# Optimization experiments

Hardware: AMD Instinct MI355X
Metric: run time of the kernel (lower is better)

The kernel has to match this reference:

```python
import jax, jax.numpy as jnp
import numpy as np

NUM_HEADS = 8  # from init_kwargs


def setup_inputs() -> dict:
    key = jax.random.key(0)
    ks = jax.random.split(key, 8)
    B, N, Din, H, Dout, E = 4, 2048, 256, 512, 256, 65536
    s = 0.02
    return {
        "x": jax.random.normal(ks[0], (B, N, Din), jnp.float32),
        "edge_index": jax.random.randint(ks[1], (2, E), 0, N),
        "W_gcn": jax.random.normal(ks[2], (Din, H), jnp.float32) * s,
        "b_gcn": jnp.zeros((H,), jnp.float32),
        "in_proj_w": jax.random.normal(ks[3], (3 * H, H), jnp.float32) * s,
        "in_proj_b": jnp.zeros((3 * H,), jnp.float32),
        "out_proj_w": jax.random.normal(ks[4], (H, H), jnp.float32) * s,
        "out_proj_b": jnp.zeros((H,), jnp.float32),
        "fc_w": jax.random.normal(ks[5], (H, Dout), jnp.float32) * s,
        "fc_b": jnp.zeros((Dout,), jnp.float32),
    }


def _gcn(x, edge_index, W, b):
    # PyG GCNConv: add self-loops, symmetric normalization, gather-scatter aggregation.
    B, N, _ = x.shape
    loop = jnp.arange(N)
    src = jnp.concatenate([edge_index[0], loop])  # message source j
    dst = jnp.concatenate([edge_index[1], loop])  # aggregation target i
    deg = jnp.zeros((N,), x.dtype).at[dst].add(1.0)
    dinv = jnp.where(deg > 0, jax.lax.rsqrt(deg), 0.0)
    norm = dinv[src] * dinv[dst]                  # [Etot]
    xl = x @ W                                    # [B, N, H]
    msgs = xl[:, src, :] * norm[None, :, None]    # [B, Etot, H]
    out = jnp.zeros_like(xl).at[:, dst].add(msgs)  # scatter-add over edges
    return out + b


def _mha(x_nbh, wi, bi, wo, bo, nh):
    # torch MultiheadAttention, input [N(seq), B, H], self-attention.
    N, B, H = x_nbh.shape
    dh = H // nh
    qkv = x_nbh @ wi.T + bi                       # [N, B, 3H]
    q, k, v = jnp.split(qkv, 3, axis=-1)
    q = q.reshape(N, B, nh, dh) * (dh ** -0.5)
    k = k.reshape(N, B, nh, dh)
    v = v.reshape(N, B, nh, dh)
    scores = jnp.einsum("nbhd,mbhd->bhnm", q, k)  # [B, nh, N, N]
    attn = jax.nn.softmax(scores, axis=-1)
    o = jnp.einsum("bhnm,mbhd->nbhd", attn, v).reshape(N, B, H)
    return o @ wo.T + bo


def reference(x, edge_index, W_gcn, b_gcn, in_proj_w, in_proj_b,
              out_proj_w, out_proj_b, fc_w, fc_b):
    h = _gcn(x, edge_index, W_gcn, b_gcn)         # [B, N, H]
    h = jnp.transpose(h, (1, 0, 2))               # [N, B, H]
    h = _mha(h, in_proj_w, in_proj_b, out_proj_w, out_proj_b, NUM_HEADS)
    h = jnp.transpose(h, (1, 0, 2))               # [B, N, H]
    h = jax.nn.relu(h)
    return h @ fc_w + fc_b                        # [B, N, Dout]
```

## Files before the change

kernel.cpp:

```cpp
#include <hip/hip_runtime.h>
#include <hip/hip_bf16.h>


#define NN 2048
#define HH 512
#define NHEAD 8
#define DH 64

typedef _Float16 f16;
typedef __attribute__((ext_vector_type(2))) _Float16 f16x2;
typedef __attribute__((ext_vector_type(4))) _Float16 f16x4;
typedef __attribute__((ext_vector_type(8))) _Float16 f16x8;
typedef __attribute__((ext_vector_type(4))) float f32x4;

#define GLOAD_LDS16(g, l)                                              \
  __builtin_amdgcn_global_load_lds(                                    \
      (const __attribute__((address_space(1))) void*)(g),              \
      (__attribute__((address_space(3))) void*)(l), 16, 0, 0)

__device__ __forceinline__ float fast_exp2(float x) {
#if __has_builtin(__builtin_amdgcn_exp2f)
  return __builtin_amdgcn_exp2f(x);
#else
  return exp2f(x);
#endif
}

__device__ __forceinline__ f16x2 cvt_pk_f16(float a, float b) {
#if __has_builtin(__builtin_amdgcn_cvt_pkrtz)
  return __builtin_bit_cast(f16x2, __builtin_amdgcn_cvt_pkrtz(a, b));
#else
  f16x2 r = { (f16)a, (f16)b };
  return r;
#endif
}


__global__ __launch_bounds__(256) void prep_all_kernel(const float* __restrict__ wi,
                                                       const float* __restrict__ wo,
                                                       const float* __restrict__ wg,
                                                       const float* __restrict__ fcw,
                                                       f16* __restrict__ wi16,
                                                       f16* __restrict__ wo16,
                                                       f16* __restrict__ wg16t,
                                                       f16* __restrict__ fcw16t,
                                                       float* __restrict__ deg,
                                                       int* __restrict__ cursor) {
  __shared__ float tbuf[32][33];
  const int bid = blockIdx.x, t = threadIdx.x;
  if (bid < 768) {
    const int i = bid * 256 + t;
    const float4 v = ((const float4*)wi)[i];
    f16x4 o = { (f16)v.x, (f16)v.y, (f16)v.z, (f16)v.w };
    ((f16x4*)wi16)[i] = o;
  } else if (bid < 1024) {
    const int i = (bid - 768) * 256 + t;
    const float4 v = ((const float4*)wo)[i];
    f16x4 o = { (f16)v.x, (f16)v.y, (f16)v.z, (f16)v.w };
    ((f16x4*)wo16)[i] = o;
  } else if (bid == 1024) {
    for (int i = t; i < NN; i += 256) { deg[i] = 0.0f; cursor[i] = 0; }
  } else {
    const int id = bid - 1025;
    const float* in;
    f16* outp;
    int R, C, bx, by;
    if (id < 128) { in = wg;  outp = wg16t;  R = 256; C = 512;
                    bx = id & 15; by = id >> 4; }
    else { int id2 = id - 128; in = fcw; outp = fcw16t; R = 512; C = 256;
           bx = id2 & 7; by = id2 >> 3; }
    const int c0 = bx * 32, r0 = by * 32;
    const int tx = t & 31, ty = t >> 5;
#pragma unroll
    for (int i = 0; i < 32; i += 8) tbuf[ty + i][tx] = in[(size_t)(r0 + ty + i) * C + c0 + tx];
    __syncthreads();
#pragma unroll
    for (int i = 0; i < 32; i += 8)
      outp[(size_t)(c0 + ty + i) * R + r0 + tx] = (f16)tbuf[tx][ty + i];
  }
}


__global__ __launch_bounds__(256) void count_deg_kernel(const int* __restrict__ ei, int E,
                                                        float* __restrict__ deg) {
  int e = blockIdx.x * 256 + threadIdx.x;
  if (e < E) atomicAdd(&deg[ei[E + e]], 1.0f);
}

__global__ __launch_bounds__(1024) void build_rowptr_kernel(const float* __restrict__ deg,
                                                            float* __restrict__ dinv,
                                                            int* __restrict__ rowptr) {
  __shared__ int a[NN];
  __shared__ int bbuf[NN];
  const int t = threadIdx.x;
  for (int i = t; i < NN; i += 1024) {
    float dg = deg[i];
    a[i] = (int)dg;
    dinv[i] = rsqrtf(dg + 1.0f);
  }
  __syncthreads();
  int* src = a;
  int* dst = bbuf;
  for (int off = 1; off < NN; off <<= 1) {
    for (int i = t; i < NN; i += 1024) {
      int v = src[i];
      if (i >= off) v += src[i - off];
      dst[i] = v;
    }
    __syncthreads();
    int* tmp = src; src = dst; dst = tmp;
  }
  for (int i = t; i < NN; i += 1024) rowptr[i + 1] = src[i];
  if (t == 0) rowptr[0] = 0;
}

__global__ __launch_bounds__(256) void fill_csr_kernel(const int* __restrict__ ei, int E,
                                                       const int* __restrict__ rowptr,
                                                       int* __restrict__ cursor,
                                                       int* __restrict__ csr_src) {
  int e = blockIdx.x * 256 + threadIdx.x;
  if (e < E) {
    int s = ei[e];
    int d = ei[E + e];
    int pos = atomicAdd(&cursor[d], 1);
    csr_src[rowptr[d] + pos] = s;
  }
}


template <int OUTMODE, bool BIAS, bool RELU, bool AF32, int MT = 128>
__global__ __launch_bounds__(256) void mfma_gemm_kernel(
    const void* __restrict__ Ap, const f16* __restrict__ Bt,
    const float* __restrict__ bias, void* __restrict__ Cout,
    int M, int N, int K,
    f16* __restrict__ q_out, f16* __restrict__ k_out, f16* __restrict__ v_out) {
  constexpr int MI = MT / 32;
  __shared__ f16 As[MT * 32];
  __shared__ f16 Bs[128 * 32];
  const int tid = threadIdx.x;
  const int wave = tid >> 6, lane = tid & 63;
  const int quad = lane >> 4, l16 = lane & 15;
  const int m0 = blockIdx.y * MT, n0 = blockIdx.x * 128;
  const int moff = (wave >> 1) * (MI * 16), noff = (wave & 1) * 64;

  f32x4 acc[MI][4];
#pragma unroll
  for (int i = 0; i < MI; ++i)
#pragma unroll
    for (int j = 0; j < 4; ++j) acc[i][j] = (f32x4){0.f, 0.f, 0.f, 0.f};

  const int rpw = MT / 4;
  const int srowA = rpw * wave + (lane >> 2);
  const int srowB = 32 * wave + (lane >> 2);
  const int kch = (lane & 3) * 8;
  const f16* Ag = (const f16*)Ap + (size_t)(m0 + srowA) * K + kch;
  const float* Ag32 = (const float*)Ap + (size_t)(m0 + srowA) * K + kch;
  const f16* Bg = Bt + (size_t)(n0 + srowB) * K + kch;
  f16* As_w = &As[(rpw * wave) * 32];
  f16* Bs_w = &Bs[(32 * wave) * 32];

  for (int k0 = 0; k0 < K; k0 += 32) {
    __syncthreads();
    if (AF32) {
#pragma unroll
      for (int t = 0; t < 2; ++t) {
        const float* g = Ag32 + k0 + (size_t)(16 * t) * K;
        const float4 u0 = *(const float4*)g;
        const float4 u1 = *(const float4*)(g + 4);
        f16x8 o = { (f16)u0.x, (f16)u0.y, (f16)u0.z, (f16)u0.w,
                    (f16)u1.x, (f16)u1.y, (f16)u1.z, (f16)u1.w };
        *(f16x8*)&As[(srowA + 16 * t) * 32 + kch] = o;
      }
    } else {
      GLOAD_LDS16(Ag + k0, As_w);
      if (MT == 128) GLOAD_LDS16(Ag + k0 + (size_t)16 * K, As_w + 16 * 32);
    }
    GLOAD_LDS16(Bg + k0, Bs_w);
    GLOAD_LDS16(Bg + k0 + (size_t)16 * K, Bs_w + 16 * 32);
    __syncthreads();
    f16x8 af[MI], bf[4];
#pragma unroll
    for (int m16 = 0; m16 < MI; ++m16)
      af[m16] = *(const f16x8*)&As[(moff + m16 * 16 + l16) * 32 + quad * 8];
#pragma unroll
    for (int n16 = 0; n16 < 4; ++n16)
      bf[n16] = *(const f16x8*)&Bs[(noff + n16 * 16 + l16) * 32 + quad * 8];
#pragma unroll
    for (int m16 = 0; m16 < MI; ++m16)
#pragma unroll
      for (int n16 = 0; n16 < 4; ++n16)
        acc[m16][n16] =
            __builtin_amdgcn_mfma_f32_16x16x32_f16(af[m16], bf[n16], acc[m16][n16], 0, 0, 0);
  }

  float bv[4];
#pragma unroll
  for (int n16 = 0; n16 < 4; ++n16)
    bv[n16] = BIAS ? bias[n0 + noff + n16 * 16 + l16] : 0.f;

  if (OUTMODE == 2) {
    const int hblk = (n0 >> 6) + (wave & 1);
    const int which = hblk >> 3, h = hblk & 7;
    f16* dst = (which == 0) ? q_out : (which == 1) ? k_out : v_out;
    const float scale = (which == 0) ? 0.125f * 1.44269504088896340736f : 1.0f;
#pragma unroll
    for (int m16 = 0; m16 < MI; ++m16) {
#pragma unroll
      for (int r = 0; r < 4; ++r) {
        const int m = m0 + moff + m16 * 16 + quad * 4 + r;
        const int b = m >> 11, ns = m & 2047;
        f16* row = dst + ((size_t)(b * 8 + h) * NN + ns) * DH;
#pragma unroll
        for (int n16 = 0; n16 < 4; ++n16) {
          const int d = n16 * 16 + l16;
          row[d] = (f16)((acc[m16][n16][r] + bv[n16]) * scale);
        }
      }
    }
  } else {
#pragma unroll
    for (int m16 = 0; m16 < MI; ++m16) {
#pragma unroll
      for (int r = 0; r < 4; ++r) {
        const size_t row = (size_t)(m0 + moff + m16 * 16 + quad * 4 + r) * N;
#pragma unroll
        for (int n16 = 0; n16 < 4; ++n16) {
          const int col = n0 + noff + n16 * 16 + l16;
          float v = acc[m16][n16][r] + bv[n16];
          if (RELU) v = fmaxf(v, 0.f);
          if (OUTMODE == 0) ((float*)Cout)[row + col] = v;
          else ((f16*)Cout)[row + col] = (f16)v;
        }
      }
    }
  }
}


__global__ __launch_bounds__(256) void gcn_aggregate_kernel(const f16* __restrict__ xl,
                                                            const float* __restrict__ dinv,
                                                            const int* __restrict__ rowptr,
                                                            const int* __restrict__ csr_src,
                                                            const float* __restrict__ b_gcn,
                                                            f16* __restrict__ out) {
  __shared__ int s_src[256];
  __shared__ float s_dv[256];
  const int i = blockIdx.x;
  const int tid = threadIdx.x;
  const float dv_i = dinv[i];
  const int b = tid >> 6;
  const int f = (tid & 63) * 8;
  const f16* xb = xl + (size_t)(b * NN) * HH + f;
  float acc[8];
  {
    const f16x8 self = *(const f16x8*)&xb[(size_t)i * HH];
#pragma unroll
    for (int j = 0; j < 8; ++j) acc[j] = (float)self[j] * dv_i;
  }
  const int beg = rowptr[i], end = rowptr[i + 1];
  for (int c0 = beg; c0 < end; c0 += 256) {
    const int cnt = min(256, end - c0);
    __syncthreads();
    if (tid < cnt) {
      int s = csr_src[c0 + tid];
      s_src[tid] = s;
      s_dv[tid] = dinv[s];
    }
    __syncthreads();
    for (int t = 0; t < cnt; ++t) {
      const f16x8 v = *(const f16x8*)&xb[(size_t)s_src[t] * HH];
      const float w = s_dv[t];
#pragma unroll
      for (int j = 0; j < 8; ++j) acc[j] = fmaf((float)v[j], w, acc[j]);
    }
  }
  const float4 bg0 = *(const float4*)&b_gcn[f];
  const float4 bg1 = *(const float4*)&b_gcn[f + 4];
  f16x8 o;
  o[0] = (f16)(acc[0] * dv_i + bg0.x);
  o[1] = (f16)(acc[1] * dv_i + bg0.y);
  o[2] = (f16)(acc[2] * dv_i + bg0.z);
  o[3] = (f16)(acc[3] * dv_i + bg0.w);
  o[4] = (f16)(acc[4] * dv_i + bg1.x);
  o[5] = (f16)(acc[5] * dv_i + bg1.y);
  o[6] = (f16)(acc[6] * dv_i + bg1.z);
  o[7] = (f16)(acc[7] * dv_i + bg1.w);
  *(f16x8*)&out[((size_t)(b * NN) + i) * HH + f] = o;
}


__global__ __launch_bounds__(256, 2) void flash_attn_f16_kernel(const f16* __restrict__ Qb,
                                                                const f16* __restrict__ Kb,
                                                                const f16* __restrict__ Vb,
                                                                f16* __restrict__ out) {
  constexpr int LDK = 72;
  constexpr int LDV = 128;
  __shared__ f16 Ks[128 * LDK];
  __shared__ f16 Vt[64 * LDV];
  const int tid = threadIdx.x;
  const int wave = tid >> 6, lane = tid & 63;
  const int quad = lane >> 4, l16 = lane & 15;
  const int bid = blockIdx.x;
  const int sw = (bid & 7) * 64 + (bid >> 3);
  const int bh = sw >> 4;
  const int n0 = (sw & 15) * 128;
  const int b = bh >> 3, h = bh & 7;
  const f16* kb = Kb + (size_t)bh * NN * DH;
  const f16* vb = Vb + (size_t)bh * NN * DH;

  f16x8 aq[2][2];
#pragma unroll
  for (int g = 0; g < 2; ++g) {
    const f16* qf = Qb + ((size_t)bh * NN + n0 + (wave + 4 * g) * 16 + l16) * DH + quad * 8;
    aq[g][0] = *(const f16x8*)qf;
    aq[g][1] = *(const f16x8*)(qf + 32);
  }

  const f16x8 ones = { (f16)1.f, (f16)1.f, (f16)1.f, (f16)1.f,
                       (f16)1.f, (f16)1.f, (f16)1.f, (f16)1.f };

  f32x4 acc_l[2];
  f32x4 acc_o[2][4];
#pragma unroll
  for (int g = 0; g < 2; ++g) {
    acc_l[g] = (f32x4){0.f, 0.f, 0.f, 0.f};
#pragma unroll
    for (int n16 = 0; n16 < 4; ++n16) acc_o[g][n16] = (f32x4){0.f, 0.f, 0.f, 0.f};
  }

  const int kr = tid >> 3, kc = (tid & 7) * 8;
  const int vdg = tid & 15, jbb = tid >> 4;
  int fdr[4];
#pragma unroll
  for (int n16 = 0; n16 < 4; ++n16)
    fdr[n16] = (2 * n16 + l16 + (l16 >> 3)) & 7;

  f16x8 kreg[4];
  f16x4 vreg[2][4];

  auto load_tile = [&](int k0) {
#pragma unroll
    for (int i = 0; i < 4; ++i)
      kreg[i] = *(const f16x8*)(kb + (size_t)(k0 + kr + 32 * i) * DH + kc);
#pragma unroll
    for (int cc = 0; cc < 2; ++cc) {
      const int jb = jbb + 16 * cc;
#pragma unroll
      for (int i = 0; i < 4; ++i)
        vreg[cc][i] = *(const f16x4*)(vb + (size_t)(k0 + jb * 4 + i) * DH + vdg * 4);
    }
  };
  auto store_tile = [&]() {
#pragma unroll
    for (int i = 0; i < 4; ++i)
      *(f16x8*)&Ks[(kr + 32 * i) * LDK + kc] = kreg[i];
#pragma unroll
    for (int cc = 0; cc < 2; ++cc) {
      const int jb = jbb + 16 * cc;
      const int vch = (jb >> 3) * 4 + (jb & 3);
      const int vrem = ((jb >> 2) & 1) * 4;
#pragma unroll
      for (int c = 0; c < 4; ++c) {
        const int d = vdg * 4 + c;
        const int fd = (d + (d >> 3)) & 7;
        const int off = (((vch & 8) | ((vch ^ fd) & 7)) << 3) + vrem;
        f16x4 o = { vreg[cc][0][c], vreg[cc][1][c], vreg[cc][2][c], vreg[cc][3][c] };
        *(f16x4*)&Vt[d * LDV + off] = o;
      }
    }
  };
  auto do_p = [&](int p) {
    f32x4 sA[2][2];
#pragma unroll
    for (int t = 0; t < 2; ++t) {
      const f16x8 ak0 = *(const f16x8*)&Ks[(p * 32 + t * 16 + l16) * LDK + quad * 8];
      const f16x8 ak1 = *(const f16x8*)&Ks[(p * 32 + t * 16 + l16) * LDK + quad * 8 + 32];
#pragma unroll
      for (int g = 0; g < 2; ++g) {
        f32x4 s = {0.f, 0.f, 0.f, 0.f};
        s = __builtin_amdgcn_mfma_f32_16x16x32_f16(ak0, aq[g][0], s, 0, 0, 0);
        s = __builtin_amdgcn_mfma_f32_16x16x32_f16(ak1, aq[g][1], s, 0, 0, 0);
        sA[g][t] = s;
      }
    }
    f16x8 bvv[4];
    const int chp = p * 4 + quad;
#pragma unroll
    for (int n16 = 0; n16 < 4; ++n16) {
      const int off = ((chp & 8) | ((chp ^ fdr[n16]) & 7)) << 3;
      bvv[n16] = *(const f16x8*)&Vt[(n16 * 16 + l16) * LDV + off];
    }
#pragma unroll
    for (int g = 0; g < 2; ++g) {
      union { f16x8 v; f16x2 hh[4]; } ap;
#pragma unroll
      for (int t = 0; t < 2; ++t)
#pragma unroll
        for (int rr = 0; rr < 2; ++rr) {
          const float e0 = fast_exp2(sA[g][t][rr * 2]);
          const float e1 = fast_exp2(sA[g][t][rr * 2 + 1]);
          ap.hh[t * 2 + rr] = cvt_pk_f16(e0, e1);
        }
      acc_l[g] = __builtin_amdgcn_mfma_f32_16x16x32_f16(ap.v, ones, acc_l[g], 0, 0, 0);
#pragma unroll
      for (int n16 = 0; n16 < 4; ++n16)
        acc_o[g][n16] = __builtin_amdgcn_mfma_f32_16x16x32_f16(ap.v, bvv[n16], acc_o[g][n16], 0, 0, 0);
    }
  };

  load_tile(0);
  store_tile();
  __syncthreads();
  for (int kt = 0; kt < NN / 128; ++kt) {
    const bool pf = (kt + 1) < (NN / 128);
    if (pf) load_tile((kt + 1) * 128);
    __builtin_amdgcn_s_setprio(1);
    do_p(0);
    do_p(1);
    do_p(2);
    do_p(3);
    __builtin_amdgcn_s_setprio(0);
    __syncthreads();
    if (pf) {
      store_tile();
      __syncthreads();
    }
  }

#pragma unroll
  for (int g = 0; g < 2; ++g) {
    f16* obase = out + ((size_t)b * NN + n0 + (wave + 4 * g) * 16) * HH + h * DH;
#pragma unroll
    for (int r = 0; r < 4; ++r) {
      const float inv = 1.0f / acc_l[g][r];
#pragma unroll
      for (int n16 = 0; n16 < 4; ++n16)
        obase[(size_t)(quad * 4 + r) * HH + n16 * 16 + l16] = (f16)(acc_o[g][n16][r] * inv);
    }
  }
}


extern "C" void kernel_launch(void* const* d_in, const int* in_sizes, int n_in,
                              void* d_out, int out_size, void* d_ws, size_t ws_size,
                              hipStream_t stream) {
  const float* x     = (const float*)d_in[0];
  const int*   ei    = (const int*)d_in[1];
  const float* W_gcn = (const float*)d_in[2];
  const float* b_gcn = (const float*)d_in[3];
  const float* wi    = (const float*)d_in[4];
  const float* bi    = (const float*)d_in[5];
  const float* wo    = (const float*)d_in[6];
  const float* bo    = (const float*)d_in[7];
  const float* fcw   = (const float*)d_in[8];
  const float* fcb   = (const float*)d_in[9];
  float* out = (float*)d_out;
  const int E = in_sizes[1] / 2;
  const int M = 4 * NN;

  char* wsb = (char*)d_ws;
  const size_t MB = 1u << 20;
  f16* xl16   = (f16*)(wsb + 4 * MB);
  f16* hb16   = (f16*)(wsb + 12 * MB);
  f16* Qb     = (f16*)(wsb + 20 * MB);
  f16* Kb     = (f16*)(wsb + 28 * MB);
  f16* Vb     = (f16*)(wsb + 36 * MB);
  f16* attn16 = (f16*)(wsb + 44 * MB);
  f16* proj16 = (f16*)(wsb + 52 * MB);
  f16* wi16   = (f16*)(wsb + 60 * MB);
  f16* wo16   = (f16*)(wsb + 62 * MB);
  f16* wg16t  = (f16*)(wsb + 63 * MB);
  f16* fcw16t = (f16*)(wsb + 64 * MB);
  float* deg  = (float*)(wsb + 65 * MB);
  float* dinv = deg + NN;
  int* rowptr = (int*)(dinv + NN);
  int* cursor = rowptr + 2080;
  int* csr    = cursor + NN;

  prep_all_kernel<<<1281, 256, 0, stream>>>(wi, wo, W_gcn, fcw, wi16, wo16,
                                            wg16t, fcw16t, deg, cursor);

  count_deg_kernel<<<(E + 255) / 256, 256, 0, stream>>>(ei, E, deg);
  build_rowptr_kernel<<<1, 1024, 0, stream>>>(deg, dinv, rowptr);
  fill_csr_kernel<<<(E + 255) / 256, 256, 0, stream>>>(ei, E, rowptr, cursor, csr);

  mfma_gemm_kernel<1, false, false, true><<<dim3(4, 64), 256, 0, stream>>>(
      x, wg16t, nullptr, xl16, M, 512, 256, nullptr, nullptr, nullptr);
  gcn_aggregate_kernel<<<NN, 256, 0, stream>>>(xl16, dinv, rowptr, csr, b_gcn, hb16);
  mfma_gemm_kernel<2, true, false, false><<<dim3(12, 64), 256, 0, stream>>>(
      hb16, wi16, bi, nullptr, M, 1536, 512, Qb, Kb, Vb);
  flash_attn_f16_kernel<<<512, 256, 0, stream>>>(Qb, Kb, Vb, attn16);
  mfma_gemm_kernel<1, true, true, false><<<dim3(4, 64), 256, 0, stream>>>(
      attn16, wo16, bo, proj16, M, 512, 512, nullptr, nullptr, nullptr);
  mfma_gemm_kernel<0, true, false, false, 64><<<dim3(2, 128), 256, 0, stream>>>(
      proj16, fcw16t, fcb, out, M, 256, 512, nullptr, nullptr, nullptr);
}
```

Measured before the change: 235.3 us.

## Double query tile per attention block and double-buffer K/V in LDS

Each flash-attention block now processes 256 query rows instead of 128, halving the grid and reusing every loaded K/V tile across twice as many queries. K and V shared-memory tiles are double-buffered so the next tile is stored into the alternate buffer, removing one barrier per iteration. The cost is more accumulator registers, one block per CU (launch bounds lowered), and less parallelism to hide latency.

```diff
diff --git a/kernel.cpp b/kernel.cpp
--- a/kernel.cpp
+++ b/kernel.cpp
@@ -289,28 +289,28 @@
 }
 
 
-__global__ __launch_bounds__(256, 2) void flash_attn_f16_kernel(const f16* __restrict__ Qb,
+__global__ __launch_bounds__(256, 1) void flash_attn_f16_kernel(const f16* __restrict__ Qb,
                                                                 const f16* __restrict__ Kb,
                                                                 const f16* __restrict__ Vb,
                                                                 f16* __restrict__ out) {
   constexpr int LDK = 72;
   constexpr int LDV = 128;
-  __shared__ f16 Ks[128 * LDK];
-  __shared__ f16 Vt[64 * LDV];
+  __shared__ f16 Ks[2][128 * LDK];
+  __shared__ f16 Vt[2][64 * LDV];
   const int tid = threadIdx.x;
   const int wave = tid >> 6, lane = tid & 63;
   const int quad = lane >> 4, l16 = lane & 15;
   const int bid = blockIdx.x;
-  const int sw = (bid & 7) * 64 + (bid >> 3);
-  const int bh = sw >> 4;
-  const int n0 = (sw & 15) * 128;
+  const int sw = (bid & 7) * 32 + (bid >> 3);
+  const int bh = sw >> 3;
+  const int n0 = (sw & 7) * 256;
   const int b = bh >> 3, h = bh & 7;
   const f16* kb = Kb + (size_t)bh * NN * DH;
   const f16* vb = Vb + (size_t)bh * NN * DH;
 
-  f16x8 aq[2][2];
-#pragma unroll
-  for (int g = 0; g < 2; ++g) {
+  f16x8 aq[4][2];
+#pragma unroll
+  for (int g = 0; g < 4; ++g) {
     const f16* qf = Qb + ((size_t)bh * NN + n0 + (wave + 4 * g) * 16 + l16) * DH + quad * 8;
     aq[g][0] = *(const f16x8*)qf;
     aq[g][1] = *(const f16x8*)(qf + 32);
@@ -319,10 +319,10 @@
   const f16x8 ones = { (f16)1.f, (f16)1.f, (f16)1.f, (f16)1.f,
                        (f16)1.f, (f16)1.f, (f16)1.f, (f16)1.f };
 
-  f32x4 acc_l[2];
-  f32x4 acc_o[2][4];
-#pragma unroll
-  for (int g = 0; g < 2; ++g) {
+  f32x4 acc_l[4];
+  f32x4 acc_o[4][4];
+#pragma unroll
+  for (int g = 0; g < 4; ++g) {
     acc_l[g] = (f32x4){0.f, 0.f, 0.f, 0.f};
 #pragma unroll
     for (int n16 = 0; n16 < 4; ++n16) acc_o[g][n16] = (f32x4){0.f, 0.f, 0.f, 0.f};
@@ -350,10 +350,10 @@
         vreg[cc][i] = *(const f16x4*)(vb + (size_t)(k0 + jb * 4 + i) * DH + vdg * 4);
     }
   };
-  auto store_tile = [&]() {
+  auto store_tile = [&](int buf) {
 #pragma unroll
     for (int i = 0; i < 4; ++i)
-      *(f16x8*)&Ks[(kr + 32 * i) * LDK + kc] = kreg[i];
+      *(f16x8*)&Ks[buf][(kr + 32 * i) * LDK + kc] = kreg[i];
 #pragma unroll
     for (int cc = 0; cc < 2; ++cc) {
       const int jb = jbb + 16 * cc;
@@ -365,18 +365,18 @@
         const int fd = (d + (d >> 3)) & 7;
         const int off = (((vch & 8) | ((vch ^ fd) & 7)) << 3) + vrem;
         f16x4 o = { vreg[cc][0][c], vreg[cc][1][c], vreg[cc][2][c], vreg[cc][3][c] };
-        *(f16x4*)&Vt[d * LDV + off] = o;
+        *(f16x4*)&Vt[buf][d * LDV + off] = o;
       }
     }
   };
-  auto do_p = [&](int p) {
-    f32x4 sA[2][2];
+  auto do_p = [&](int p, const f16* KsC, const f16* VtC) {
+    f32x4 sA[4][2];
 #pragma unroll
     for (int t = 0; t < 2; ++t) {
-      const f16x8 ak0 = *(const f16x8*)&Ks[(p * 32 + t * 16 + l16) * LDK + quad * 8];
-      const f16x8 ak1 = *(const f16x8*)&Ks[(p * 32 + t * 16 + l16) * LDK + quad * 8 + 32];
-#pragma unroll
-      for (int g = 0; g < 2; ++g) {
+      const f16x8 ak0 = *(const f16x8*)&KsC[(p * 32 + t * 16 + l16) * LDK + quad * 8];
+      const f16x8 ak1 = *(const f16x8*)&KsC[(p * 32 + t * 16 + l16) * LDK + quad * 8 + 32];
+#pragma unroll
+      for (int g = 0; g < 4; ++g) {
         f32x4 s = {0.f, 0.f, 0.f, 0.f};
         s = __builtin_amdgcn_mfma_f32_16x16x32_f16(ak0, aq[g][0], s, 0, 0, 0);
         s = __builtin_amdgcn_mfma_f32_16x16x32_f16(ak1, aq[g][1], s, 0, 0, 0);
@@ -388,10 +388,10 @@
 #pragma unroll
     for (int n16 = 0; n16 < 4; ++n16) {
       const int off = ((chp & 8) | ((chp ^ fdr[n16]) & 7)) << 3;
-      bvv[n16] = *(const f16x8*)&Vt[(n16 * 16 + l16) * LDV + off];
-    }
-#pragma unroll
-    for (int g = 0; g < 2; ++g) {
+      bvv[n16] = *(const f16x8*)&VtC[(n16 * 16 + l16) * LDV + off];
+    }
+#pragma unroll
+    for (int g = 0; g < 4; ++g) {
       union { f16x8 v; f16x2 hh[4]; } ap;
 #pragma unroll
       for (int t = 0; t < 2; ++t)
@@ -409,26 +409,26 @@
   };
 
   load_tile(0);
-  store_tile();
-  __syncthreads();
+  store_tile(0);
+  int cur = 0;
   for (int kt = 0; kt < NN / 128; ++kt) {
+    __syncthreads();
     const bool pf = (kt + 1) < (NN / 128);
     if (pf) load_tile((kt + 1) * 128);
+    const f16* KsC = &Ks[cur][0];
+    const f16* VtC = &Vt[cur][0];
     __builtin_amdgcn_s_setprio(1);
-    do_p(0);
-    do_p(1);
-    do_p(2);
-    do_p(3);
+    do_p(0, KsC, VtC);
+    do_p(1, KsC, VtC);
+    do_p(2, KsC, VtC);
+    do_p(3, KsC, VtC);
     __builtin_amdgcn_s_setprio(0);
-    __syncthreads();
-    if (pf) {
-      store_tile();
-      __syncthreads();
-    }
-  }
-
-#pragma unroll
-  for (int g = 0; g < 2; ++g) {
+    if (pf) store_tile(cur ^ 1);
+    cur ^= 1;
+  }
+
+#pragma unroll
+  for (int g = 0; g < 4; ++g) {
     f16* obase = out + ((size_t)b * NN + n0 + (wave + 4 * g) * 16) * HH + h * DH;
 #pragma unroll
     for (int r = 0; r < 4; ++r) {
@@ -489,7 +489,7 @@
   gcn_aggregate_kernel<<<NN, 256, 0, stream>>>(xl16, dinv, rowptr, csr, b_gcn, hb16);
   mfma_gemm_kernel<2, true, false, false><<<dim3(12, 64), 256, 0, stream>>>(
       hb16, wi16, bi, nullptr, M, 1536, 512, Qb, Kb, Vb);
-  flash_attn_f16_kernel<<<512, 256, 0, stream>>>(Qb, Kb, Vb, attn16);
+  flash_attn_f16_kernel<<<256, 256, 0, stream>>>(Qb, Kb, Vb, attn16);
   mfma_gemm_kernel<1, true, true, false><<<dim3(4, 64), 256, 0, stream>>>(
       attn16, wo16, bo, proj16, M, 512, 512, nullptr, nullptr, nullptr);
   mfma_gemm_kernel<0, true, false, false, 64><<<dim3(2, 128), 256, 0, stream>>>(
```

After: 241.4 us. 1.03x slower.

## Double GEMM K-tile to 64 and XOR-swizzle LDS layout

Applied to the files above, without the earlier changes.

The MFMA GEMM kernel now stages a K-depth of 64 per iteration instead of 32, halving the number of barrier-separated load/compute steps. Global loads are remapped so each wave loads 8 rows per instruction with an XOR-swizzled 16-byte chunk index, and the fragment reads apply the same swizzle to avoid LDS bank conflicts. This doubles LDS usage per block, which may reduce occupancy, and the f32 A path writes unswizzled positions while loading from swizzled global offsets, so the two must stay consistent.

```diff
diff --git a/kernel.cpp b/kernel.cpp
--- a/kernel.cpp
+++ b/kernel.cpp
@@ -135,8 +135,9 @@
     int M, int N, int K,
     f16* __restrict__ q_out, f16* __restrict__ k_out, f16* __restrict__ v_out) {
   constexpr int MI = MT / 32;
-  __shared__ f16 As[MT * 32];
-  __shared__ f16 Bs[128 * 32];
+  constexpr int BK = 64;
+  __shared__ f16 As[MT * BK];
+  __shared__ f16 Bs[128 * BK];
   const int tid = threadIdx.x;
   const int wave = tid >> 6, lane = tid & 63;
   const int quad = lane >> 4, l16 = lane & 15;
@@ -150,47 +151,57 @@
     for (int j = 0; j < 4; ++j) acc[i][j] = (f32x4){0.f, 0.f, 0.f, 0.f};
 
   const int rpw = MT / 4;
-  const int srowA = rpw * wave + (lane >> 2);
-  const int srowB = 32 * wave + (lane >> 2);
-  const int kch = (lane & 3) * 8;
-  const f16* Ag = (const f16*)Ap + (size_t)(m0 + srowA) * K + kch;
-  const float* Ag32 = (const float*)Ap + (size_t)(m0 + srowA) * K + kch;
-  const f16* Bg = Bt + (size_t)(n0 + srowB) * K + kch;
-  f16* As_w = &As[(rpw * wave) * 32];
-  f16* Bs_w = &Bs[(32 * wave) * 32];
-
-  for (int k0 = 0; k0 < K; k0 += 32) {
+  const int srow8 = lane >> 3;
+  const int kchsw = (((lane & 7) ^ srow8) * 8);
+  const f16* Ag = (const f16*)Ap + (size_t)(m0 + rpw * wave + srow8) * K + kchsw;
+  const float* Ag32 = (const float*)Ap + (size_t)(m0 + rpw * wave + srow8) * K + kchsw;
+  const f16* Bg = Bt + (size_t)(n0 + 32 * wave + srow8) * K + kchsw;
+  f16* As_w = &As[(rpw * wave) * BK];
+  f16* Bs_w = &Bs[(32 * wave) * BK];
+
+  for (int k0 = 0; k0 < K; k0 += BK) {
     __syncthreads();
     if (AF32) {
 #pragma unroll
-      for (int t = 0; t < 2; ++t) {
-        const float* g = Ag32 + k0 + (size_t)(16 * t) * K;
+      for (int i = 0; i < rpw / 8; ++i) {
+        const float* g = Ag32 + k0 + (size_t)(8 * i) * K;
         const float4 u0 = *(const float4*)g;
         const float4 u1 = *(const float4*)(g + 4);
         f16x8 o = { (f16)u0.x, (f16)u0.y, (f16)u0.z, (f16)u0.w,
                     (f16)u1.x, (f16)u1.y, (f16)u1.z, (f16)u1.w };
-        *(f16x8*)&As[(srowA + 16 * t) * 32 + kch] = o;
+        *(f16x8*)&As[(rpw * wave + 8 * i + srow8) * BK + (lane & 7) * 8] = o;
       }
     } else {
-      GLOAD_LDS16(Ag + k0, As_w);
-      if (MT == 128) GLOAD_LDS16(Ag + k0 + (size_t)16 * K, As_w + 16 * 32);
-    }
-    GLOAD_LDS16(Bg + k0, Bs_w);
-    GLOAD_LDS16(Bg + k0 + (size_t)16 * K, Bs_w + 16 * 32);
-    __syncthreads();
-    f16x8 af[MI], bf[4];
-#pragma unroll
-    for (int m16 = 0; m16 < MI; ++m16)
-      af[m16] = *(const f16x8*)&As[(moff + m16 * 16 + l16) * 32 + quad * 8];
-#pragma unroll
-    for (int n16 = 0; n16 < 4; ++n16)
-      bf[n16] = *(const f16x8*)&Bs[(noff + n16 * 16 + l16) * 32 + quad * 8];
-#pragma unroll
-    for (int m16 = 0; m16 < MI; ++m16)
-#pragma unroll
-      for (int n16 = 0; n16 < 4; ++n16)
-        acc[m16][n16] =
-            __builtin_amdgcn_mfma_f32_16x16x32_f16(af[m16], bf[n16], acc[m16][n16], 0, 0, 0);
+#pragma unroll
+      for (int i = 0; i < rpw / 8; ++i)
+        GLOAD_LDS16(Ag + k0 + (size_t)(8 * i) * K, As_w + (8 * i) * BK);
+    }
+#pragma unroll
+    for (int i = 0; i < 4; ++i)
+      GLOAD_LDS16(Bg + k0 + (size_t)(8 * i) * K, Bs_w + (8 * i) * BK);
+    __syncthreads();
+#pragma unroll
+    for (int kk = 0; kk < 2; ++kk) {
+      f16x8 af[MI], bf[4];
+#pragma unroll
+      for (int m16 = 0; m16 < MI; ++m16) {
+        const int r = moff + m16 * 16 + l16;
+        const int ch = (4 * kk + quad) ^ (r & 7);
+        af[m16] = *(const f16x8*)&As[r * BK + ch * 8];
+      }
+#pragma unroll
+      for (int n16 = 0; n16 < 4; ++n16) {
+        const int r = noff + n16 * 16 + l16;
+        const int ch = (4 * kk + quad) ^ (r & 7);
+        bf[n16] = *(const f16x8*)&Bs[r * BK + ch * 8];
+      }
+#pragma unroll
+      for (int m16 = 0; m16 < MI; ++m16)
+#pragma unroll
+        for (int n16 = 0; n16 < 4; ++n16)
+          acc[m16][n16] =
+              __builtin_amdgcn_mfma_f32_16x16x32_f16(af[m16], bf[n16], acc[m16][n16], 0, 0, 0);
+    }
   }
 
   float bv[4];
```

After: 229.8 us. -2.4%, faster.
